# Performance work log

Measured on AMD Instinct MI355X. Metric: run time of the kernel, lower is better.

The kernel has to match this reference:

```python
import jax, jax.numpy as jnp
import numpy as np
import math

B, S, E = 4, 2048, 1024
H, D = 16, 64

def setup_inputs() -> dict:
    key = jax.random.key(0)
    ks = jax.random.split(key, 9)
    sE = 1.0 / math.sqrt(E)
    sHD = 1.0 / math.sqrt(H * D)
    return {
        "x": jax.random.normal(ks[0], (B, S, E), jnp.float32),
        "Wq": jax.random.normal(ks[1], (H, E, D), jnp.float32) * sE,
        "bq": jax.random.normal(ks[2], (H, D), jnp.float32) * sE,
        "Wk": jax.random.normal(ks[3], (H, E, D), jnp.float32) * sE,
        "bk": jax.random.normal(ks[4], (H, D), jnp.float32) * sE,
        "Wv": jax.random.normal(ks[5], (H, E, D), jnp.float32) * sE,
        "bv": jax.random.normal(ks[6], (H, D), jnp.float32) * sE,
        "Wo": jax.random.normal(ks[7], (E, E), jnp.float32) * sHD,
        "bo": jax.random.normal(ks[8], (E,), jnp.float32) * sHD,
    }

def reference(x, Wq, bq, Wk, bk, Wv, bv, Wo, bo):
    # Projections for all heads at once: [B,H,S,D]
    Q = jnp.einsum('bse,hed->bhsd', x, Wq) + bq[:, None, :]
    K = jnp.einsum('bse,hed->bhsd', x, Wk) + bk[:, None, :]
    V = jnp.einsum('bse,hed->bhsd', x, Wv) + bv[:, None, :]
    scale = 1.0 / math.sqrt(D)
    scores = jnp.einsum('bhsd,bhtd->bhst', Q, K) * scale  # [B,H,S,S]
    S_len = x.shape[1]
    causal = jnp.tril(jnp.ones((S_len, S_len), dtype=bool))
    scores = jnp.where(causal, scores, -jnp.inf)
    probs = jax.nn.softmax(scores, axis=-1)
    ctx = jnp.einsum('bhst,bhtd->bhsd', probs, V)  # [B,H,S,D]
    # concat heads: head order matches torch cat over ModuleList
    conc = jnp.transpose(ctx, (0, 2, 1, 3)).reshape(x.shape[0], S_len, H * D)
    # torch Linear: y = conc @ W.T + b ; Wo stored as [out,in]=[E,E]
    out = conc @ Wo.T + bo
    # dropout is identity in eval mode
    return out
```

## Files before the change

### kernel.cpp

```cpp
#include <hip/hip_runtime.h>
#include <math.h>

constexpr int Bn = 4;
constexpr int Sn = 2048;
constexpr int En = 1024;
constexpr int Hn = 16;
constexpr int Dn = 64;

typedef float f32x4 __attribute__((ext_vector_type(4)));
typedef short s16x8 __attribute__((ext_vector_type(8)));
typedef short s16x4 __attribute__((ext_vector_type(4)));

__device__ __forceinline__ short f2bf(float f) {
    unsigned u = __builtin_bit_cast(unsigned, f);
    unsigned r = (u + 0x7fffu + ((u >> 16) & 1u)) >> 16;
    return (short)r;
}

__device__ __forceinline__ void glds16(const short* g, short* l) {
    __builtin_amdgcn_global_load_lds(
        (const __attribute__((address_space(1))) short*)g,
        (__attribute__((address_space(3))) short*)l, 16, 0, 0);
}

__global__ __launch_bounds__(256) void conv_x_kernel(
    const float* __restrict__ x, short* __restrict__ y)
{
    size_t i = ((size_t)blockIdx.x * 256 + threadIdx.x) * 4;
    float4 v = *(const float4*)(x + i);
    s16x4 o;
    o[0] = f2bf(v.x); o[1] = f2bf(v.y); o[2] = f2bf(v.z); o[3] = f2bf(v.w);
    *(s16x4*)(y + i) = o;
}

__global__ __launch_bounds__(256) void build_wcat_kernel(
    const float* __restrict__ Wq, const float* __restrict__ bq,
    const float* __restrict__ Wk, const float* __restrict__ bk,
    const float* __restrict__ Wv, const float* __restrict__ bv,
    short* __restrict__ Wcat, float* __restrict__ bias_cat)
{
    const int et = blockIdx.x, h = blockIdx.y, p = blockIdx.z;
    const float* W  = (p == 0) ? Wq : (p == 1) ? Wk : Wv;
    const float* bb = (p == 0) ? bq : (p == 1) ? bk : bv;
    const float* Wh = W + (size_t)h * En * Dn;

    __shared__ float T[64][65];
    const int tid = threadIdx.x;
    #pragma unroll
    for (int it = 0; it < 16; it++) {
        int idx = tid + it * 256;
        int e = idx >> 6, d = idx & 63;
        T[d][e] = Wh[(size_t)(et * 64 + e) * Dn + d];
    }
    __syncthreads();
    #pragma unroll
    for (int it = 0; it < 16; it++) {
        int idx = tid + it * 256;
        int d = idx >> 6, e = idx & 63;
        Wcat[(size_t)(p * 1024 + h * 64 + d) * En + et * 64 + e] = f2bf(T[d][e]);
    }
    if (et == 0 && tid < 64)
        bias_cat[p * 1024 + h * 64 + tid] = bb[h * 64 + tid];
}

__global__ __launch_bounds__(256) void conv_wo_kernel(
    const float* __restrict__ Wo, short* __restrict__ Wob)
{
    const size_t base = (size_t)blockIdx.x * En;
    #pragma unroll
    for (int i = 0; i < 4; i++) {
        int k = threadIdx.x + i * 256;
        Wob[base + k] = f2bf(Wo[base + k]);
    }
}

__global__ __launch_bounds__(512) void gemm_bt_kernel(
    const short* __restrict__ A,
    const short* __restrict__ Bt,
    const float* __restrict__ bias,
    float* __restrict__ outF,
    short* __restrict__ Qb, short* __restrict__ Kb, short* __restrict__ Vtb,
    int mode)
{
    constexpr int K = En;
    const int m0 = blockIdx.x * 256;
    const int n0 = blockIdx.y * 128;

    __shared__ short As[256 * 64];
    __shared__ short Bs[128 * 64];

    const int tid  = threadIdx.x;
    const int w    = tid >> 6;
    const int lane = tid & 63;
    const int quad = lane >> 4;
    const int l15  = lane & 15;
    const int wr = (w >> 1) * 64;
    const int wc = (w & 1) * 64;

    f32x4 acc[4][4];
    #pragma unroll
    for (int i = 0; i < 4; i++)
        #pragma unroll
        for (int j = 0; j < 4; j++)
            #pragma unroll
            for (int e = 0; e < 4; e++) acc[i][j][e] = 0.f;

    for (int k0 = 0; k0 < K; k0 += 64) {
        #pragma unroll
        for (int r = 0; r < 4; r++) {
            int c   = (r * 8 + w) * 64 + lane;
            int row = c >> 3;
            int lp  = (c & 7) ^ (row & 7);
            glds16(A + (size_t)(m0 + row) * K + k0 + lp * 8,
                   As + (r * 8 + w) * 512);
        }
        #pragma unroll
        for (int r = 0; r < 2; r++) {
            int c   = (r * 8 + w) * 64 + lane;
            int row = c >> 3;
            int lp  = (c & 7) ^ (row & 7);
            glds16(Bt + (size_t)(n0 + row) * K + k0 + lp * 8,
                   Bs + (r * 8 + w) * 512);
        }
        __syncthreads();

        #pragma unroll
        for (int ks = 0; ks < 2; ks++) {
            s16x8 af[4], bfr[4];
            #pragma unroll
            for (int mt = 0; mt < 4; mt++) {
                int row = wr + mt * 16 + l15;
                af[mt] = *(const s16x8*)&As[row * 64 + (((ks * 4 + quad) ^ (l15 & 7)) * 8)];
            }
            #pragma unroll
            for (int nt = 0; nt < 4; nt++) {
                int row = wc + nt * 16 + l15;
                bfr[nt] = *(const s16x8*)&Bs[row * 64 + (((ks * 4 + quad) ^ (l15 & 7)) * 8)];
            }
            #pragma unroll
            for (int mt = 0; mt < 4; mt++)
                #pragma unroll
                for (int nt = 0; nt < 4; nt++)
                    acc[mt][nt] = __builtin_amdgcn_mfma_f32_16x16x32_bf16(
                        af[mt], bfr[nt], acc[mt][nt], 0, 0, 0);
        }
        __syncthreads();
    }

    if (mode == 0) {
        #pragma unroll
        for (int mt = 0; mt < 4; mt++) {
            #pragma unroll
            for (int reg = 0; reg < 4; reg++) {
                int m = m0 + wr + mt * 16 + quad * 4 + reg;
                #pragma unroll
                for (int nt = 0; nt < 4; nt++) {
                    int n = n0 + wc + nt * 16 + l15;
                    outF[(size_t)m * En + n] = acc[mt][nt][reg] + bias[n];
                }
            }
        }
    } else {
        const int p = (n0 + wc) >> 10;
        if (p < 2) {
            const float qs = (p == 0) ? 0.18033688011112042f : 1.0f;
            short* dst = (p == 0) ? Qb : Kb;
            #pragma unroll
            for (int mt = 0; mt < 4; mt++) {
                #pragma unroll
                for (int reg = 0; reg < 4; reg++) {
                    int m = m0 + wr + mt * 16 + quad * 4 + reg;
                    int b = m >> 11, s = m & 2047;
                    #pragma unroll
                    for (int nt = 0; nt < 4; nt++) {
                        int n = n0 + wc + nt * 16 + l15;
                        int h = (n >> 6) & 15, d = n & 63;
                        dst[(((size_t)(b * Hn + h)) * Sn + s) * Dn + d] =
                            f2bf((acc[mt][nt][reg] + bias[n]) * qs);
                    }
                }
            }
        } else {
            #pragma unroll
            for (int mt = 0; mt < 4; mt++) {
                int m = m0 + wr + mt * 16 + quad * 4;
                int b = m >> 11, s = m & 2047;
                #pragma unroll
                for (int nt = 0; nt < 4; nt++) {
                    int n = n0 + wc + nt * 16 + l15;
                    int h = (n >> 6) & 15, d = n & 63;
                    s16x4 pk;
                    #pragma unroll
                    for (int reg = 0; reg < 4; reg++)
                        pk[reg] = f2bf(acc[mt][nt][reg] + bias[n]);
                    *(s16x4*)(Vtb + (((size_t)(b * Hn + h)) * Dn + d) * Sn + s) = pk;
                }
            }
        }
    }
}

__global__ __launch_bounds__(512) void attn_mfma_kernel(
    const short* __restrict__ Q, const short* __restrict__ K,
    const short* __restrict__ Vt, short* __restrict__ Cb)
{
    constexpr int PP = 72;
    const int i  = blockIdx.x;
    const int bh = blockIdx.y;
    const int b = bh >> 4, hh = bh & 15;
    const int t0 = i, t1 = 31 - i;

    __shared__ short SMEM[17408];
    __shared__ float l_sh[2][128];
    short* Ks  = SMEM;
    short* Vts = SMEM + 4096;
    short* Ps  = SMEM + 8192;

    const int tid  = threadIdx.x;
    const int w5   = tid >> 6;
    const int lane = tid & 63;
    const int quad = lane >> 4;
    const int l15  = lane & 15;
    const int ws = w5 & 3;
    const int h  = w5 >> 2;

    const short* Kp = K + (size_t)bh * Sn * Dn;
    const short* Vp = Vt + (size_t)bh * Dn * Sn;

    const int tf[2] = {t0, t1};
    s16x8 aq[2][2];
    #pragma unroll
    for (int f = 0; f < 2; f++)
        #pragma unroll
        for (int ks = 0; ks < 2; ks++)
            aq[f][ks] = *(const s16x8*)(
                Q + ((size_t)bh * Sn + tf[f] * 64 + ws * 16 + l15) * Dn +
                ks * 32 + quad * 8);

    f32x4 acc[2][4];
    #pragma unroll
    for (int f = 0; f < 2; f++)
        #pragma unroll
        for (int nt = 0; nt < 4; nt++)
            #pragma unroll
            for (int e = 0; e < 4; e++) acc[f][nt][e] = 0.f;
    float lpart[2] = {0.f, 0.f};

    for (int kt = 0; kt <= t1; kt++) {
        {
            int c   = w5 * 64 + lane;
            int row = c >> 3;
            int lp  = (c & 7) ^ (row & 7);
            glds16(Kp + (size_t)(kt * 64 + row) * Dn + lp * 8, Ks + w5 * 512);
            glds16(Vp + (size_t)row * Sn + kt * 64 + lp * 8, Vts + w5 * 512);
        }
        __syncthreads();

        #pragma unroll
        for (int f = 0; f < 2; f++) {
            if (kt > tf[f]) continue;
            f32x4 st[2];
            #pragma unroll
            for (int ntl = 0; ntl < 2; ntl++)
                #pragma unroll
                for (int e = 0; e < 4; e++) st[ntl][e] = 0.f;
            #pragma unroll
            for (int ks = 0; ks < 2; ks++) {
                #pragma unroll
                for (int ntl = 0; ntl < 2; ntl++) {
                    int nt = h * 2 + ntl;
                    s16x8 bk = *(const s16x8*)&Ks[(nt * 16 + l15) * 64 +
                                                  (((ks * 4 + quad) ^ (l15 & 7)) * 8)];
                    st[ntl] = __builtin_amdgcn_mfma_f32_16x16x32_bf16(
                        bk, aq[f][ks], st[ntl], 0, 0, 0);
                }
            }
            const bool diag = (kt == tf[f]);
            #pragma unroll
            for (int ntl = 0; ntl < 2; ntl++) {
                int nt = h * 2 + ntl;
                unsigned tb[4];
                #pragma unroll
                for (int reg = 0; reg < 4; reg++) {
                    float v = __builtin_amdgcn_exp2f(st[ntl][reg]);
                    if (diag && (nt * 16 + quad * 4 + reg) > (ws * 16 + l15))
                        v = 0.f;
                    lpart[f] += v;
                    tb[reg] = __builtin_bit_cast(unsigned, v);
                }
                uint2 pk;
                pk.x = (tb[0] >> 16) | (tb[1] & 0xFFFF0000u);
                pk.y = (tb[2] >> 16) | (tb[3] & 0xFFFF0000u);
                *(uint2*)&Ps[(f * 64 + ws * 16 + l15) * PP + nt * 16 + quad * 4] = pk;
            }
        }

        s16x8 bv[4];
        #pragma unroll
        for (int nt = 0; nt < 4; nt++)
            bv[nt] = *(const s16x8*)&Vts[(nt * 16 + l15) * 64 +
                                         (((h * 4 + quad) ^ (l15 & 7)) * 8)];
        #pragma unroll
        for (int f = 0; f < 2; f++) {
            if (kt > tf[f]) continue;
            s16x8 ap = *(const s16x8*)&Ps[(f * 64 + ws * 16 + l15) * PP +
                                          h * 32 + quad * 8];
            #pragma unroll
            for (int nt = 0; nt < 4; nt++)
                acc[f][nt] = __builtin_amdgcn_mfma_f32_16x16x32_bf16(
                    ap, bv[nt], acc[f][nt], 0, 0, 0);
        }
        __syncthreads();
    }

    #pragma unroll
    for (int f = 0; f < 2; f++) {
        float l = lpart[f];
        l += __shfl_xor(l, 16);
        l += __shfl_xor(l, 32);
        if (quad == 0) l_sh[h][f * 64 + ws * 16 + l15] = l;
    }
    float* Obuf = (float*)SMEM;
    if (h == 1) {
        #pragma unroll
        for (int f = 0; f < 2; f++)
            #pragma unroll
            for (int nt = 0; nt < 4; nt++)
                #pragma unroll
                for (int reg = 0; reg < 4; reg++)
                    Obuf[(f * 64 + ws * 16 + quad * 4 + reg) * 65 + nt * 16 + l15] =
                        acc[f][nt][reg];
    }
    __syncthreads();
    if (h == 0) {
        #pragma unroll
        for (int f = 0; f < 2; f++) {
            #pragma unroll
            for (int reg = 0; reg < 4; reg++) {
                int row = ws * 16 + quad * 4 + reg;
                int s = tf[f] * 64 + row;
                float linv = 1.f / (l_sh[0][f * 64 + row] + l_sh[1][f * 64 + row]);
                #pragma unroll
                for (int nt = 0; nt < 4; nt++) {
                    float o = acc[f][nt][reg] + Obuf[(f * 64 + row) * 65 + nt * 16 + l15];
                    Cb[((size_t)(b * Sn + s)) * En + hh * 64 + nt * 16 + l15] =
                        f2bf(o * linv);
                }
            }
        }
    }
}

extern "C" void kernel_launch(void* const* d_in, const int* in_sizes, int n_in,
                              void* d_out, int out_size, void* d_ws, size_t ws_size,
                              hipStream_t stream) {
    const float* x  = (const float*)d_in[0];
    const float* Wq = (const float*)d_in[1];
    const float* bq = (const float*)d_in[2];
    const float* Wk = (const float*)d_in[3];
    const float* bk = (const float*)d_in[4];
    const float* Wv = (const float*)d_in[5];
    const float* bv = (const float*)d_in[6];
    const float* Wo = (const float*)d_in[7];
    const float* bo = (const float*)d_in[8];
    float* out = (float*)d_out;

    const size_t XS   = (size_t)Bn * Sn * En;
    const size_t WCS  = (size_t)3 * En * Hn * Dn;
    const size_t WOS  = (size_t)En * En;
    const size_t QSZ  = (size_t)Bn * Hn * Sn * Dn;

    short* Ax    = (short*)d_ws;
    short* Wcat  = Ax + XS;
    short* Wob   = Wcat + WCS;
    float* biasc = (float*)(Wob + WOS);
    short* Qb    = (short*)(biasc + 3072);
    short* Kb    = Qb + QSZ;
    short* Vtb   = Kb + QSZ;
    short* Cbf   = Vtb + QSZ;

    conv_x_kernel<<<dim3(XS / (256 * 4)), 256, 0, stream>>>(x, Ax);
    build_wcat_kernel<<<dim3(16, 16, 3), 256, 0, stream>>>(Wq, bq, Wk, bk, Wv, bv,
                                                           Wcat, biasc);
    conv_wo_kernel<<<dim3(En), 256, 0, stream>>>(Wo, Wob);

    gemm_bt_kernel<<<dim3((Bn * Sn) / 256, 3072 / 128), 512, 0, stream>>>(
        Ax, Wcat, biasc, nullptr, Qb, Kb, Vtb, 1);

    attn_mfma_kernel<<<dim3(16, Bn * Hn), 512, 0, stream>>>(Qb, Kb, Vtb, Cbf);

    gemm_bt_kernel<<<dim3((Bn * Sn) / 256, En / 128), 512, 0, stream>>>(
        Cbf, Wob, bo, out, nullptr, nullptr, nullptr, 0);
}
```

Baseline: 260.8 us.

## Load K/V fragments directly from global into registers, dropping LDS staging

The attention loop no longer stages each 64-row K tile and transposed V tile into shared memory with global_load_lds. Each wave now reads its own MFMA operand fragments straight from global memory, so both per-iteration __syncthreads can go, since the P buffer is written and read only by the same wave. A single barrier is added after the loop because the output buffer aliases the P buffer. The cost is that each K/V element is fetched by several waves through the cache instead of once, and global-load latency sits directly in front of the MFMAs with no prefetch.

```diff
diff --git a/kernel.cpp b/kernel.cpp
--- a/kernel.cpp
+++ b/kernel.cpp
@@ -210,11 +210,9 @@
     const int b = bh >> 4, hh = bh & 15;
     const int t0 = i, t1 = 31 - i;
 
-    __shared__ short SMEM[17408];
+    __shared__ short SMEM[16640];
     __shared__ float l_sh[2][128];
-    short* Ks  = SMEM;
-    short* Vts = SMEM + 4096;
-    short* Ps  = SMEM + 8192;
+    short* Ps = SMEM;
 
     const int tid  = threadIdx.x;
     const int w5   = tid >> 6;
@@ -247,14 +245,20 @@
     float lpart[2] = {0.f, 0.f};
 
     for (int kt = 0; kt <= t1; kt++) {
-        {
-            int c   = w5 * 64 + lane;
-            int row = c >> 3;
-            int lp  = (c & 7) ^ (row & 7);
-            glds16(Kp + (size_t)(kt * 64 + row) * Dn + lp * 8, Ks + w5 * 512);
-            glds16(Vp + (size_t)row * Sn + kt * 64 + lp * 8, Vts + w5 * 512);
-        }
-        __syncthreads();
+        s16x8 bk[2][2];
+        #pragma unroll
+        for (int ks = 0; ks < 2; ks++)
+            #pragma unroll
+            for (int ntl = 0; ntl < 2; ntl++) {
+                int nt = h * 2 + ntl;
+                bk[ks][ntl] = *(const s16x8*)(
+                    Kp + (size_t)(kt * 64 + nt * 16 + l15) * Dn + ks * 32 + quad * 8);
+            }
+        s16x8 bv[4];
+        #pragma unroll
+        for (int nt = 0; nt < 4; nt++)
+            bv[nt] = *(const s16x8*)(
+                Vp + (size_t)(nt * 16 + l15) * Sn + kt * 64 + h * 32 + quad * 8);
 
         #pragma unroll
         for (int f = 0; f < 2; f++) {
@@ -265,16 +269,12 @@
                 #pragma unroll
                 for (int e = 0; e < 4; e++) st[ntl][e] = 0.f;
             #pragma unroll
-            for (int ks = 0; ks < 2; ks++) {
-                #pragma unroll
-                for (int ntl = 0; ntl < 2; ntl++) {
-                    int nt = h * 2 + ntl;
-                    s16x8 bk = *(const s16x8*)&Ks[(nt * 16 + l15) * 64 +
-                                                  (((ks * 4 + quad) ^ (l15 & 7)) * 8)];
+            for (int ks = 0; ks < 2; ks++)
+                #pragma unroll
+                for (int ntl = 0; ntl < 2; ntl++)
                     st[ntl] = __builtin_amdgcn_mfma_f32_16x16x32_bf16(
-                        bk, aq[f][ks], st[ntl], 0, 0, 0);
-                }
-            }
+                        bk[ks][ntl], aq[f][ks], st[ntl], 0, 0, 0);
+
             const bool diag = (kt == tf[f]);
             #pragma unroll
             for (int ntl = 0; ntl < 2; ntl++) {
@@ -295,11 +295,6 @@
             }
         }
 
-        s16x8 bv[4];
-        #pragma unroll
-        for (int nt = 0; nt < 4; nt++)
-            bv[nt] = *(const s16x8*)&Vts[(nt * 16 + l15) * 64 +
-                                         (((h * 4 + quad) ^ (l15 & 7)) * 8)];
         #pragma unroll
         for (int f = 0; f < 2; f++) {
             if (kt > tf[f]) continue;
@@ -310,7 +305,6 @@
                 acc[f][nt] = __builtin_amdgcn_mfma_f32_16x16x32_bf16(
                     ap, bv[nt], acc[f][nt], 0, 0, 0);
         }
-        __syncthreads();
     }
 
     #pragma unroll
@@ -320,6 +314,8 @@
         l += __shfl_xor(l, 32);
         if (quad == 0) l_sh[h][f * 64 + ws * 16 + l15] = l;
     }
+    __syncthreads();
+
     float* Obuf = (float*)SMEM;
     if (h == 1) {
         #pragma unroll
```

New measurement: 418.9 us. +60.6%, slower.
